# Optimization experiments

Hardware: AMD Instinct MI355X
Metric: run time of the kernel (lower is better)

## Reference

```python
import jax, jax.numpy as jnp
import numpy as np

N, E, G = 50000, 600000, 500          # nodes, edges, graphs in batch
IN_NODE, HID, EDGE = 92, 64, 41       # CGCNN default feature dims
NCONV, PRED, NOUT = 3, 128, 1
Z_DIM = 2 * HID + EDGE                # 169: cat(src_x, dst_x, edge_attr)
BN_EPS = 1e-5


def setup_inputs() -> dict:
    key = jax.random.key(0)
    ks = jax.random.split(key, 14)
    f32 = jnp.float32
    return {
        "x": jax.random.normal(ks[0], (N, IN_NODE), f32),
        "edge_attr": jax.random.normal(ks[1], (E, EDGE), f32),
        "src": jax.random.randint(ks[2], (E,), 0, N),
        "dst": jax.random.randint(ks[3], (E,), 0, N),
        "graph_idx": jnp.sort(jax.random.randint(ks[4], (N,), 0, G)),
        "n_graphs": G,
        "W_embed": jax.random.normal(ks[5], (IN_NODE, HID), f32) / np.sqrt(IN_NODE),
        "b_embed": jnp.zeros((HID,), f32),
        "W_sig": jax.random.normal(ks[6], (NCONV, Z_DIM, HID), f32) / np.sqrt(Z_DIM),
        "b_sig": jnp.zeros((NCONV, HID), f32),
        "W_sp": jax.random.normal(ks[7], (NCONV, Z_DIM, HID), f32) / np.sqrt(Z_DIM),
        "b_sp": jnp.zeros((NCONV, HID), f32),
        "bn_gamma": jnp.ones((NCONV, HID), f32),
        "bn_beta": jnp.zeros((NCONV, HID), f32),
        "W_fc": jax.random.normal(ks[8], (HID, PRED), f32) / np.sqrt(HID),
        "b_fc": jnp.zeros((PRED,), f32),
        "W_out": jax.random.normal(ks[9], (PRED, NOUT), f32) / np.sqrt(PRED),
        "b_out": jnp.zeros((NOUT,), f32),
    }


def reference(x, edge_attr, src, dst, graph_idx, n_graphs,
              W_embed, b_embed, W_sig, b_sig, W_sp, b_sp,
              bn_gamma, bn_beta, W_fc, b_fc, W_out, b_out):
    # node embedding to hidden dim
    h = x @ W_embed + b_embed                                   # [N, HID]
    n_nodes = h.shape[0]
    for i in range(W_sig.shape[0]):
        # per-edge features: gather src/dst node feats + edge feats
        z = jnp.concatenate([h[src], h[dst], edge_attr], axis=1)  # [E, Z_DIM]
        gated = jax.nn.sigmoid(z @ W_sig[i] + b_sig[i])           # [E, HID]
        msg = jax.nn.softplus(z @ W_sp[i] + b_sp[i])              # [E, HID]
        # scatter-sum gated messages into destination node mailboxes
        agg = jax.ops.segment_sum(gated * msg, dst, num_segments=n_nodes)
        h = h + agg                                               # residual
        # batch norm over nodes (training-mode batch stats, biased var)
        mean = h.mean(axis=0)
        var = h.var(axis=0)
        h = (h - mean) * jax.lax.rsqrt(var + BN_EPS) * bn_gamma[i] + bn_beta[i]
    # sum-pool nodes per graph, then dense readout
    graph_feat = jax.ops.segment_sum(h, graph_idx, num_segments=n_graphs)  # [G, HID]
    graph_feat = graph_feat @ W_fc + b_fc                                  # [G, PRED]
    return graph_feat @ W_out + b_out                                      # [G, NOUT]
```

## Files before the change

### kernel.cpp

```cpp
#include <hip/hip_runtime.h>

#define N_NODES 50000
#define N_EDGES 600000
#define N_GRAPHS 500
#define IN_F 92
#define HID 64
#define EDGE_F 41
#define ZDIM 169
#define PRED 128
#define BN_EPS 1e-5f
#define SCAN_BLOCKS 196
#define ROW_U32 24
#define LOG2E 1.4426950408889634f
#define LN2   0.6931471805599453f
#define NAGG_BLOCKS 2048
#define NW2 (NAGG_BLOCKS * 8)
#define PART_T ((N_EDGES + 1 + NW2 - 1) / NW2)

typedef unsigned int u32;
typedef _Float16 f16;
typedef _Float16 f16x2 __attribute__((ext_vector_type(2)));
typedef _Float16 f16x8 __attribute__((ext_vector_type(8)));
typedef float f32x4 __attribute__((ext_vector_type(4)));

__device__ __forceinline__ u32 f2bf(float f) {
    u32 u = __float_as_uint(f);
    return (u + 0x7fffu + ((u >> 16) & 1u)) >> 16;
}

__device__ __forceinline__ int lbound(const int* __restrict__ a, int nelem, int val) {
    int lo = 0, hi = nelem;
    while (lo < hi) {
        int m = (lo + hi) >> 1;
        if (a[m] < val) lo = m + 1; else hi = m;
    }
    return lo;
}

__global__ void k_zeroAll(int* __restrict__ ip, int n1, float* __restrict__ fp, int n2) {
    int i = blockIdx.x * 256 + threadIdx.x;
    if (i < n1) ip[i] = 0;
    else if (i - n1 < n2) fp[i - n1] = 0.f;
}

__global__ void k_hist(const int* __restrict__ dst, int* __restrict__ deg) {
    int e = blockIdx.x * 256 + threadIdx.x;
    if (e < N_EDGES) atomicAdd(&deg[dst[e]], 1);
}

__global__ __launch_bounds__(256) void k_scanA(const int* __restrict__ deg,
                                               int* __restrict__ partial) {
    __shared__ int s[256];
    int i = blockIdx.x * 256 + threadIdx.x;
    s[threadIdx.x] = (i < N_NODES) ? deg[i] : 0;
    __syncthreads();
    for (int off = 128; off > 0; off >>= 1) {
        if (threadIdx.x < off) s[threadIdx.x] += s[threadIdx.x + off];
        __syncthreads();
    }
    if (threadIdx.x == 0) partial[blockIdx.x] = s[0];
}

__global__ __launch_bounds__(256) void k_scanB(const int* __restrict__ partial,
                                               int* __restrict__ partialExc,
                                               int* __restrict__ rowptr) {
    __shared__ int s[256];
    int t = threadIdx.x;
    int v = (t < SCAN_BLOCKS) ? partial[t] : 0;
    s[t] = v;
    __syncthreads();
    for (int off = 1; off < 256; off <<= 1) {
        int x = (t >= off) ? s[t - off] : 0;
        __syncthreads();
        s[t] += x;
        __syncthreads();
    }
    partialExc[t] = s[t] - v;
    if (t == 0) rowptr[N_NODES] = N_EDGES;
}

__global__ __launch_bounds__(256) void k_scanC(const int* __restrict__ deg,
                                               const int* __restrict__ partialExc,
                                               int* __restrict__ rowptr) {
    __shared__ int s[256];
    int i = blockIdx.x * 256 + threadIdx.x;
    int t = threadIdx.x;
    int v = (i < N_NODES) ? deg[i] : 0;
    s[t] = v;
    __syncthreads();
    for (int off = 1; off < 256; off <<= 1) {
        int x = (t >= off) ? s[t - off] : 0;
        __syncthreads();
        s[t] += x;
        __syncthreads();
    }
    if (i < N_NODES) rowptr[i] = s[t] - v + partialExc[blockIdx.x];
}

__global__ void k_part(const int* __restrict__ rowptr, int* __restrict__ partW) {
    int i = blockIdx.x * 256 + threadIdx.x;
    if (i <= NW2) partW[i] = min(lbound(rowptr, N_NODES + 1, i * PART_T), N_NODES);
}

__global__ void k_rank(const int* __restrict__ dst, const int* __restrict__ src,
                       const int* __restrict__ rowptr, int* __restrict__ cursor,
                       int* __restrict__ srcS, int* __restrict__ iperm) {
    int e = blockIdx.x * 256 + threadIdx.x;
    if (e >= N_EDGES) {
        if (e < N_EDGES + 32) srcS[e] = 0;
        return;
    }
    int d = dst[e];
    int p = rowptr[d] + atomicAdd(&cursor[d], 1);
    srcS[p] = src[e];
    iperm[p] = e;
}

__global__ __launch_bounds__(256) void k_epackS(const float* __restrict__ ea,
                                                const int* __restrict__ iperm,
                                                u32* __restrict__ eapS) {
    const int total = N_EDGES * ROW_U32;
    const int stride = gridDim.x * 256;
    for (int idx = blockIdx.x * 256 + threadIdx.x; idx < total; idx += stride) {
        int p = idx / ROW_U32;
        int q = idx - p * ROW_U32;
        int e = iperm[p];
        int k0 = 2 * q, k1 = k0 + 1;
        float f0 = (k0 < EDGE_F) ? ea[(size_t)e * EDGE_F + k0] : 0.f;
        float f1 = (k1 < EDGE_F) ? ea[(size_t)e * EDGE_F + k1] : 0.f;
        f16x2 hv = {(f16)f0, (f16)f1};
        eapS[idx] = __builtin_bit_cast(u32, hv);
    }
}

__global__ void k_wprepAll(const float* __restrict__ Wsig, const float* __restrict__ Wsp,
                           const float* __restrict__ Wemb,
                           f16* __restrict__ Wf16, f16* __restrict__ Wp2,
                           f16* __restrict__ Wef) {
    int t = blockIdx.x * 256 + threadIdx.x;
    if (t < 3072) {
        int lane = t & 63;
        int jt = (t >> 6) & 7;
        int kt = (t >> 9) & 1;
        int L = t >> 10;
        int j128 = jt * 16 + (lane & 15);
        const float* Wbase = (j128 < 64) ? Wsig : Wsp;
        int j = j128 & 63;
        f16x8 v;
        #pragma unroll
        for (int b = 0; b < 8; ++b) {
            int k = kt * 32 + (lane >> 4) * 8 + b;
            float f = (k < EDGE_F) ? Wbase[(size_t)L * ZDIM * HID + (128 + k) * HID + j] * LOG2E : 0.f;
            v[b] = (f16)f;
        }
        *(f16x8*)(Wf16 + ((size_t)((L * 2 + kt) * 8 + jt) * 64 + lane) * 8) = v;
    } else if (t < 9216) {
        int t2 = t - 3072;
        int lane = t2 & 63;
        int jt = (t2 >> 6) & 15;
        int kt = (t2 >> 10) & 1;
        int L = t2 >> 11;
        int j256 = jt * 16 + (lane & 15);
        const float* Wbase = (j256 & 64) ? Wsp : Wsig;
        int rowoff = (j256 & 128) ? 64 : 0;
        int j = j256 & 63;
        f16x8 v;
        #pragma unroll
        for (int b = 0; b < 8; ++b) {
            int k = kt * 32 + (lane >> 4) * 8 + b;
            v[b] = (f16)Wbase[(size_t)L * ZDIM * HID + (rowoff + k) * HID + j];
        }
        *(f16x8*)(Wp2 + ((size_t)((L * 2 + kt) * 16 + jt) * 64 + lane) * 8) = v;
    } else if (t < 9984) {
        int t3 = t - 9216;
        int lane = t3 & 63;
        int jt = (t3 >> 6) & 3;
        int kt = t3 >> 8;
        int j = jt * 16 + (lane & 15);
        f16x8 v;
        #pragma unroll
        for (int b = 0; b < 8; ++b) {
            int k = kt * 32 + (lane >> 4) * 8 + b;
            v[b] = (k < IN_F) ? (f16)Wemb[(size_t)k * HID + j] : (f16)0.f;
        }
        *(f16x8*)(Wef + ((size_t)(kt * 4 + jt) * 64 + lane) * 8) = v;
    }
}

__global__ __launch_bounds__(256) void k_embedm(const float* __restrict__ x,
                                                const f16* __restrict__ Wef,
                                                const float* __restrict__ b,
                                                float* __restrict__ A) {
    __shared__ f16x8 Wl[12 * 64];
    for (int i = threadIdx.x; i < 12 * 64; i += 256) Wl[i] = ((const f16x8*)Wef)[i];
    __syncthreads();
    const int lane = threadIdx.x & 63;
    const int col = lane & 15, grp = lane >> 4;
    float bj[4];
    #pragma unroll
    for (int jt = 0; jt < 4; ++jt) bj[jt] = b[jt * 16 + col];
    const int wid = blockIdx.x * 4 + (threadIdx.x >> 6);
    const int nw = gridDim.x * 4;
    for (int c = wid; c < N_NODES / 16; c += nw) {
        const int node = c * 16 + col;
        const float* xr = x + (size_t)node * IN_F;
        f16x8 af[3];
        #pragma unroll
        for (int kt = 0; kt < 3; ++kt) {
            int base = kt * 32 + grp * 8;
            float4 v0 = *(const float4*)(xr + base);
            float4 v1 = (base + 4 < IN_F) ? *(const float4*)(xr + base + 4)
                                          : make_float4(0.f, 0.f, 0.f, 0.f);
            af[kt] = f16x8{(f16)v0.x, (f16)v0.y, (f16)v0.z, (f16)v0.w,
                           (f16)v1.x, (f16)v1.y, (f16)v1.z, (f16)v1.w};
        }
        #pragma unroll
        for (int jt = 0; jt < 4; ++jt) {
            f32x4 c4 = {};
            c4 = __builtin_amdgcn_mfma_f32_16x16x32_f16(af[0], Wl[(0 * 4 + jt) * 64 + lane], c4, 0, 0, 0);
            c4 = __builtin_amdgcn_mfma_f32_16x16x32_f16(af[1], Wl[(1 * 4 + jt) * 64 + lane], c4, 0, 0, 0);
            c4 = __builtin_amdgcn_mfma_f32_16x16x32_f16(af[2], Wl[(2 * 4 + jt) * 64 + lane], c4, 0, 0, 0);
            #pragma unroll
            for (int r = 0; r < 4; ++r)
                A[(size_t)(c * 16 + grp * 4 + r) * HID + jt * 16 + col] = c4[r] + bj[jt];
        }
    }
}

__global__ __launch_bounds__(256, 4) void k_projm(const float* __restrict__ A,
                                                  const float* __restrict__ statsPrev,
                                                  const float* __restrict__ gammaP,
                                                  const float* __restrict__ betaP,
                                                  int applyBN,
                                                  const f16* __restrict__ Wp2L,
                                                  const float* __restrict__ bsig,
                                                  const float* __restrict__ bsp,
                                                  u32* __restrict__ pA,
                                                  u32* __restrict__ pB,
                                                  float* __restrict__ statsOut) {
    __shared__ f16x8 Wl[32 * 64];
    for (int i = threadIdx.x; i < 32 * 64; i += 256) Wl[i] = ((const f16x8*)Wp2L)[i];
    if (blockIdx.x == 0)
        for (int i = threadIdx.x; i < 128 * 32; i += 256) statsOut[i] = 0.f;
    __syncthreads();
    const int lane = threadIdx.x & 63;
    const int col = lane & 15;
    float sck[2][8], shk[2][8];
    #pragma unroll
    for (int kt = 0; kt < 2; ++kt)
        #pragma unroll
        for (int b = 0; b < 8; ++b) {
            int k = kt * 32 + (lane >> 4) * 8 + b;
            float scv = 1.f, shv = 0.f;
            if (applyBN) {
                float m = statsPrev[k * 32] * (1.f / N_NODES);
                float v = statsPrev[(64 + k) * 32] * (1.f / N_NODES) - m * m;
                scv = rsqrtf(v + BN_EPS) * gammaP[k];
                shv = betaP[k] - m * scv;
            }
            sck[kt][b] = scv;
            shk[kt][b] = shv;
        }
    float bAs[4], bPs[4];
    #pragma unroll
    for (int jt = 0; jt < 4; ++jt) {
        bAs[jt] = bsig[jt * 16 + col] * LOG2E;
        bPs[jt] = bsp[jt * 16 + col] * LOG2E;
    }
    const int wid = blockIdx.x * 4 + (threadIdx.x >> 6);
    const int nw = gridDim.x * 4;
    for (int c = wid; c < N_NODES / 16; c += nw) {
        const int node = c * 16 + col;
        const float4* Arow = (const float4*)(A + (size_t)node * HID);
        f16x8 af[2];
        #pragma unroll
        for (int kt = 0; kt < 2; ++kt) {
            float4 v0 = Arow[kt * 8 + (lane >> 4) * 2];
            float4 v1 = Arow[kt * 8 + (lane >> 4) * 2 + 1];
            float e0 = v0.x * sck[kt][0] + shk[kt][0];
            float e1 = v0.y * sck[kt][1] + shk[kt][1];
            float e2 = v0.z * sck[kt][2] + shk[kt][2];
            float e3 = v0.w * sck[kt][3] + shk[kt][3];
            float e4 = v1.x * sck[kt][4] + shk[kt][4];
            float e5 = v1.y * sck[kt][5] + shk[kt][5];
            float e6 = v1.z * sck[kt][6] + shk[kt][6];
            float e7 = v1.w * sck[kt][7] + shk[kt][7];
            af[kt] = f16x8{(f16)e0, (f16)e1, (f16)e2, (f16)e3,
                           (f16)e4, (f16)e5, (f16)e6, (f16)e7};
        }
        #pragma unroll
        for (int h = 0; h < 2; ++h) {
            f32x4 c4[8];
            #pragma unroll
            for (int jt2 = 0; jt2 < 8; ++jt2) {
                int jt = h * 8 + jt2;
                f32x4 acc = {};
                acc = __builtin_amdgcn_mfma_f32_16x16x32_f16(af[0], Wl[(0 * 16 + jt) * 64 + lane], acc, 0, 0, 0);
                c4[jt2] = __builtin_amdgcn_mfma_f32_16x16x32_f16(af[1], Wl[(1 * 16 + jt) * 64 + lane], acc, 0, 0, 0);
            }
            u32* dstArr = h ? pB : pA;
            #pragma unroll
            for (int jt2 = 0; jt2 < 4; ++jt2)
                #pragma unroll
                for (int r = 0; r < 4; ++r) {
                    float s = fmaf(c4[jt2][r], LOG2E, h ? 0.f : bAs[jt2]);
                    float p = fmaf(c4[jt2 + 4][r], LOG2E, h ? 0.f : bPs[jt2]);
                    int n2 = c * 16 + (lane >> 4) * 4 + r;
                    dstArr[(size_t)n2 * HID + jt2 * 16 + col] = f2bf(s) | (f2bf(p) << 16);
                }
        }
    }
}


#define CTX_DECL_INIT(S, widx)                                                \
    int n##S = __builtin_amdgcn_readfirstlane(partW[widx]);                   \
    const int ne##S = __builtin_amdgcn_readfirstlane(partW[(widx) + 1]);      \
    bool act##S = n##S < ne##S;                                               \
    int rb##S = 0, re##S = 0;                                                 \
    float resid##S = 0.f;                                                     \
    float bsg##S[4], bsp##S[4], accv##S[4];                                   \
    int s0##S = 0, s1##S = 0, s2##S = 0, s3##S = 0;                           \
    {                                                                         \
        _Pragma("unroll")                                                     \
        for (int jt = 0; jt < 4; ++jt) {                                      \
            bsg##S[jt] = 0.f; bsp##S[jt] = 0.f; accv##S[jt] = 0.f;            \
        }                                                                     \
        if (act##S) {                                                         \
            rb##S = __builtin_amdgcn_readfirstlane(rowptr[n##S]);             \
            re##S = __builtin_amdgcn_readfirstlane(rowptr[n##S + 1]);         \
            resid##S = A[(size_t)n##S * HID + lane];                          \
            if (applyBN) resid##S = resid##S * scL + shL;                     \
            _Pragma("unroll")                                                 \
            for (int jt = 0; jt < 4; ++jt) {                                  \
                u32 pb = pBv[(size_t)n##S * HID + jt * 16 + col];             \
                bsg##S[jt] = __uint_as_float(pb << 16);                       \
                bsp##S[jt] = __uint_as_float(pb & 0xffff0000u);               \
            }                                                                 \
            const int* sp = srcS + rb##S + rowb;                              \
            s0##S = sp[0]; s1##S = sp[1]; s2##S = sp[2]; s3##S = sp[3];       \
        }                                                                     \
    }

#define STEP_LOADS(S)                                                         \
    u32 ga##S[4][4];                                                          \
    f16x8 a0##S, a1##S;                                                       \
    if (act##S) {                                                             \
        const u32* g0##S = pAv + (size_t)s0##S * HID + col;                   \
        const u32* g1##S = pAv + (size_t)s1##S * HID + col;                   \
        const u32* g2##S = pAv + (size_t)s2##S * HID + col;                   \
        const u32* g3##S = pAv + (size_t)s3##S * HID + col;                   \
        _Pragma("unroll")                                                     \
        for (int jt = 0; jt < 4; ++jt) {                                      \
            ga##S[jt][0] = g0##S[jt * 16];                                    \
            ga##S[jt][1] = g1##S[jt * 16];                                    \
            ga##S[jt][2] = g2##S[jt * 16];                                    \
            ga##S[jt][3] = g3##S[jt * 16];                                    \
        }                                                                     \
        const f16x8* arow##S = (const f16x8*)(eapS + (size_t)(rb##S + col) * ROW_U32); \
        a0##S = arow##S[grp];                                                 \
        a1##S = arow##S[4 + grp];                                             \
    }

#define STEP_COMPUTE(S)                                                       \
    if (act##S) {                                                             \
        const int cnt##S = re##S - rb##S;                                     \
        if (cnt##S > 0) {                                                     \
            _Pragma("unroll")                                                 \
            for (int jt = 0; jt < 4; ++jt) {                                  \
                f32x4 cs = {bsg##S[jt], bsg##S[jt], bsg##S[jt], bsg##S[jt]};  \
                f32x4 cp = {bsp##S[jt], bsp##S[jt], bsp##S[jt], bsp##S[jt]};  \
                f16x8 w0s = Wlds[(jt) * 64 + lane];                           \
                f16x8 w1s = Wlds[(8 + jt) * 64 + lane];                       \
                f16x8 w0p = Wlds[(4 + jt) * 64 + lane];                       \
                f16x8 w1p = Wlds[(12 + jt) * 64 + lane];                      \
                cs = __builtin_amdgcn_mfma_f32_16x16x32_f16(a0##S, w0s, cs, 0, 0, 0); \
                cs = __builtin_amdgcn_mfma_f32_16x16x32_f16(a1##S, w1s, cs, 0, 0, 0); \
                cp = __builtin_amdgcn_mfma_f32_16x16x32_f16(a0##S, w0p, cp, 0, 0, 0); \
                cp = __builtin_amdgcn_mfma_f32_16x16x32_f16(a1##S, w1p, cp, 0, 0, 0); \
                _Pragma("unroll")                                             \
                for (int r = 0; r < 4; ++r) {                                 \
                    float s_ = cs[r] + __uint_as_float(ga##S[jt][r] << 16);   \
                    float p_ = cp[r] + __uint_as_float(ga##S[jt][r] & 0xffff0000u); \
                    float g_ = __builtin_amdgcn_rcpf(1.f + exp2f(-s_));       \
                    float m_ = fmaxf(p_, 0.f) + log2f(1.f + exp2f(-fabsf(p_))); \
                    accv##S[jt] += (rowb + r < cnt##S) ? g_ * m_ : 0.f;       \
                }                                                             \
            }                                                                 \
            rb##S += 16;                                                      \
        }                                                                     \
        while (rb##S >= re##S) {                                              \
            _Pragma("unroll")                                                 \
            for (int jt = 0; jt < 4; ++jt) {                                  \
                accv##S[jt] += __shfl_xor(accv##S[jt], 16);                   \
                accv##S[jt] += __shfl_xor(accv##S[jt], 32);                   \
            }                                                                 \
            float accSel = (lane & 32) ? ((lane & 16) ? accv##S[3] : accv##S[2]) \
                                       : ((lane & 16) ? accv##S[1] : accv##S[0]); \
            float outv = resid##S + accSel * LN2;                             \
            Aout[(size_t)n##S * HID + lane] = outv;                           \
            lsum += outv;                                                     \
            lsq += outv * outv;                                               \
            accv##S[0] = accv##S[1] = accv##S[2] = accv##S[3] = 0.f;          \
            rb##S = re##S;                                                    \
            ++n##S;                                                           \
            if (n##S >= ne##S) { act##S = false; break; }                     \
            re##S = __builtin_amdgcn_readfirstlane(rowptr[n##S + 1]);         \
            resid##S = A[(size_t)n##S * HID + lane];                          \
            if (applyBN) resid##S = resid##S * scL + shL;                     \
            _Pragma("unroll")                                                 \
            for (int jt = 0; jt < 4; ++jt) {                                  \
                u32 pb = pBv[(size_t)n##S * HID + jt * 16 + col];             \
                bsg##S[jt] = __uint_as_float(pb << 16);                       \
                bsp##S[jt] = __uint_as_float(pb & 0xffff0000u);               \
            }                                                                 \
        }                                                                     \
        if (act##S) {                                                         \
            const int* sp##S = srcS + rb##S + rowb;                           \
            s0##S = sp##S[0]; s1##S = sp##S[1];                               \
            s2##S = sp##S[2]; s3##S = sp##S[3];                               \
        }                                                                     \
    }

__global__ __launch_bounds__(256, 4) void k_nodeagg(const float* __restrict__ A,
                                                    const float* __restrict__ statsPrev,
                                                    const float* __restrict__ gammaP,
                                                    const float* __restrict__ betaP,
                                                    int applyBN,
                                                    const u32* __restrict__ pAv,
                                                    const u32* __restrict__ pBv,
                                                    const u32* __restrict__ eapS,
                                                    const int* __restrict__ srcS,
                                                    const int* __restrict__ rowptr,
                                                    const int* __restrict__ partW,
                                                    const f16* __restrict__ Wf16L,
                                                    float* __restrict__ Aout,
                                                    float* __restrict__ statsOut) {
    __shared__ f16x8 Wlds[16 * 64];
    __shared__ float redS[256], redQ[256];
    for (int i = threadIdx.x; i < 16 * 64; i += 256)
        Wlds[i] = ((const f16x8*)Wf16L)[i];

    const int lane = threadIdx.x & 63;
    const int col = lane & 15;
    const int grp = lane >> 4;
    const int rowb = grp * 4;

    float scL = 1.f, shL = 0.f;
    if (applyBN) {
        float m = statsPrev[lane * 32] * (1.f / N_NODES);
        float v = statsPrev[(64 + lane) * 32] * (1.f / N_NODES) - m * m;
        scL = rsqrtf(v + BN_EPS) * gammaP[lane];
        shL = betaP[lane] - m * scL;
    }
    __syncthreads();

    const int w2 = (((blockIdx.x << 2) + (threadIdx.x >> 6)) << 1);
    float lsum = 0.f, lsq = 0.f;

    CTX_DECL_INIT(A, w2)
    CTX_DECL_INIT(B, w2 + 1)

    while (actA || actB) {
        STEP_LOADS(A)
        STEP_LOADS(B)
        STEP_COMPUTE(A)
        STEP_COMPUTE(B)
    }

    redS[threadIdx.x] = lsum;
    redQ[threadIdx.x] = lsq;
    __syncthreads();
    if (threadIdx.x < 64) {
        float s = redS[threadIdx.x] + redS[threadIdx.x + 64] + redS[threadIdx.x + 128] + redS[threadIdx.x + 192];
        float q = redQ[threadIdx.x] + redQ[threadIdx.x + 64] + redQ[threadIdx.x + 128] + redQ[threadIdx.x + 192];
        unsafeAtomicAdd(&statsOut[threadIdx.x * 32], s);
        unsafeAtomicAdd(&statsOut[(64 + threadIdx.x) * 32], q);
    }
}

__global__ __launch_bounds__(256) void k_poolbn(const float* __restrict__ A,
                                                const float* __restrict__ stats,
                                                const float* __restrict__ gamma,
                                                const float* __restrict__ beta,
                                                const int* __restrict__ gidx,
                                                float* __restrict__ gf) {
    const int lane = threadIdx.x & 63;
    float m = stats[lane * 32] * (1.f / N_NODES);
    float v = stats[(64 + lane) * 32] * (1.f / N_NODES) - m * m;
    float scv = rsqrtf(v + BN_EPS) * gamma[lane];
    float shv = beta[lane] - m * scv;
    const int wid = blockIdx.x * 4 + (threadIdx.x >> 6);
    const int nwaves = gridDim.x * 4;
    const int chunk = (N_NODES + nwaves - 1) / nwaves;
    int r0 = wid * chunk;
    if (r0 >= N_NODES) return;
    int r1 = min(r0 + chunk, N_NODES);
    int gcur = gidx[r0];
    float acc = 0.f;
    for (int r = r0; r < r1; ++r) {
        int g = gidx[r];
        if (g != gcur) {
            unsafeAtomicAdd(&gf[(size_t)gcur * HID + lane], acc);
            acc = 0.f;
            gcur = g;
        }
        acc += A[(size_t)r * HID + lane] * scv + shv;
    }
    unsafeAtomicAdd(&gf[(size_t)gcur * HID + lane], acc);
}

__global__ __launch_bounds__(256) void k_readout(const float* __restrict__ gf,
                                                 const float* __restrict__ Wfc,
                                                 const float* __restrict__ bfc,
                                                 const float* __restrict__ Wout,
                                                 const float* __restrict__ bout,
                                                 float* __restrict__ out) {
    const int lane = threadIdx.x & 63;
    const int g = blockIdx.x * 4 + (threadIdx.x >> 6);
    if (g >= N_GRAPHS) return;
    const float* row = gf + (size_t)g * HID;
    float p0 = bfc[lane], p1 = bfc[64 + lane];
    #pragma unroll 4
    for (int k = 0; k < HID; ++k) {
        float v = row[k];
        p0 += v * Wfc[k * PRED + lane];
        p1 += v * Wfc[k * PRED + 64 + lane];
    }
    float part = p0 * Wout[lane] + p1 * Wout[64 + lane];
    #pragma unroll
    for (int off = 32; off > 0; off >>= 1) part += __shfl_xor(part, off);
    if (lane == 0) out[g] = part + bout[0];
}

extern "C" void kernel_launch(void* const* d_in, const int* in_sizes, int n_in,
                              void* d_out, int out_size, void* d_ws, size_t ws_size,
                              hipStream_t stream) {
    const float* x         = (const float*)d_in[0];
    const float* edge_attr = (const float*)d_in[1];
    const int*   src       = (const int*)d_in[2];
    const int*   dst       = (const int*)d_in[3];
    const int*   gidx      = (const int*)d_in[4];
    const float* W_embed   = (const float*)d_in[6];
    const float* b_embed   = (const float*)d_in[7];
    const float* W_sig     = (const float*)d_in[8];
    const float* b_sig     = (const float*)d_in[9];
    const float* W_sp      = (const float*)d_in[10];
    const float* b_sp      = (const float*)d_in[11];
    const float* bn_gamma  = (const float*)d_in[12];
    const float* bn_beta   = (const float*)d_in[13];
    const float* W_fc      = (const float*)d_in[14];
    const float* b_fc      = (const float*)d_in[15];
    const float* W_out     = (const float*)d_in[16];
    const float* b_out     = (const float*)d_in[17];
    float* out = (float*)d_out;

    const size_t NH = (size_t)N_NODES * HID;
    float* ws     = (float*)d_ws;
    float* A      = ws;
    u32*   pA     = (u32*)(A + NH);
    u32*   pB     = pA + NH;
    u32*   eapS   = pB + NH;
    int*   srcS   = (int*)(eapS + (size_t)(N_EDGES + 32) * ROW_U32);
    int*   iperm  = srcS + N_EDGES + 32;
    int*   rowptr = iperm + N_EDGES;
    int*   deg    = rowptr + N_NODES + 1;
    int*   cursor = deg + N_NODES;
    int*   partial    = cursor + N_NODES;
    int*   partialExc = partial + 256;
    int*   partW  = partialExc + 256;
    f16*   Wf16   = (f16*)(partW + NW2 + 2);
    f16*   Wp2    = Wf16 + 3 * 2 * 8 * 64 * 8;
    f16*   Wef    = Wp2 + 3 * 2 * 16 * 64 * 8;
    float* stats  = (float*)(Wef + 3 * 4 * 64 * 8);
    float* gf     = stats + 3 * 4096;

    k_wprepAll<<<39, 256, 0, stream>>>(W_sig, W_sp, W_embed, Wf16, Wp2, Wef);
    k_zeroAll<<<(2 * N_NODES + N_GRAPHS * HID + 255) / 256, 256, 0, stream>>>(
        deg, 2 * N_NODES, gf, N_GRAPHS * HID);
    k_hist<<<(N_EDGES + 255) / 256, 256, 0, stream>>>(dst, deg);
    k_scanA<<<SCAN_BLOCKS, 256, 0, stream>>>(deg, partial);
    k_scanB<<<1, 256, 0, stream>>>(partial, partialExc, rowptr);
    k_scanC<<<SCAN_BLOCKS, 256, 0, stream>>>(deg, partialExc, rowptr);
    k_part<<<(NW2 + 1 + 255) / 256, 256, 0, stream>>>(rowptr, partW);
    k_rank<<<(N_EDGES + 32 + 255) / 256, 256, 0, stream>>>(dst, src, rowptr, cursor, srcS, iperm);
    k_embedm<<<512, 256, 0, stream>>>(x, Wef, b_embed, A);
    k_epackS<<<4096, 256, 0, stream>>>(edge_attr, iperm, eapS);

    for (int i = 0; i < 3; ++i) {
        const float* stPrev = stats + (size_t)(i > 0 ? i - 1 : 0) * 4096;
        const float* gP     = bn_gamma + (i > 0 ? i - 1 : 0) * HID;
        const float* bP     = bn_beta + (i > 0 ? i - 1 : 0) * HID;
        float* stOut        = stats + (size_t)i * 4096;
        int applyBN = (i > 0) ? 1 : 0;
        k_projm<<<512, 256, 0, stream>>>(A, stPrev, gP, bP, applyBN,
                                         Wp2 + (size_t)i * 2 * 16 * 64 * 8,
                                         b_sig + i * HID, b_sp + i * HID,
                                         pA, pB, stOut);
        k_nodeagg<<<NAGG_BLOCKS, 256, 0, stream>>>(A, stPrev, gP, bP, applyBN,
                                                   pA, pB, eapS, srcS, rowptr, partW,
                                                   Wf16 + (size_t)i * 2 * 8 * 64 * 8,
                                                   A, stOut);
    }

    k_poolbn<<<256, 256, 0, stream>>>(A, stats + 2 * 4096, bn_gamma + 2 * HID,
                                      bn_beta + 2 * HID, gidx, gf);
    k_readout<<<(N_GRAPHS + 3) / 4, 256, 0, stream>>>(gf, W_fc, b_fc, W_out, b_out, out);
}
```

Before: 528.9 us.

## Vectorize bf16 pair layout, fuse prep/partition kernels, merge pool+readout per graph

```diff
diff --git a/kernel.cpp b/kernel.cpp
--- a/kernel.cpp
+++ b/kernel.cpp
@@ -28,6 +28,10 @@
     return (u + 0x7fffu + ((u >> 16) & 1u)) >> 16;
 }
 
+__device__ __forceinline__ u32 vget(uint4 v, int i) {
+    switch (i) { case 0: return v.x; case 1: return v.y; case 2: return v.z; default: return v.w; }
+}
+
 __device__ __forceinline__ int lbound(const int* __restrict__ a, int nelem, int val) {
     int lo = 0, hi = nelem;
     while (lo < hi) {
@@ -37,10 +41,64 @@
     return lo;
 }
 
-__global__ void k_zeroAll(int* __restrict__ ip, int n1, float* __restrict__ fp, int n2) {
-    int i = blockIdx.x * 256 + threadIdx.x;
-    if (i < n1) ip[i] = 0;
-    else if (i - n1 < n2) fp[i - n1] = 0.f;
+__global__ void k_prep(const float* __restrict__ Wsig, const float* __restrict__ Wsp,
+                       const float* __restrict__ Wemb, const int* __restrict__ gidx,
+                       f16* __restrict__ Wf16, f16* __restrict__ Wp2,
+                       f16* __restrict__ Wef, int* __restrict__ gstart,
+                       int* __restrict__ zeroBase) {
+    int t = blockIdx.x * 256 + threadIdx.x;
+    if (t < 3072) {
+        int lane = t & 63;
+        int jt = (t >> 6) & 7;
+        int kt = (t >> 9) & 1;
+        int L = t >> 10;
+        int j128 = jt * 16 + (lane & 15);
+        const float* Wbase = (j128 < 64) ? Wsig : Wsp;
+        int j = j128 & 63;
+        f16x8 v;
+        #pragma unroll
+        for (int b = 0; b < 8; ++b) {
+            int k = kt * 32 + (lane >> 4) * 8 + b;
+            float f = (k < EDGE_F) ? Wbase[(size_t)L * ZDIM * HID + (128 + k) * HID + j] * LOG2E : 0.f;
+            v[b] = (f16)f;
+        }
+        *(f16x8*)(Wf16 + ((size_t)((L * 2 + kt) * 8 + jt) * 64 + lane) * 8) = v;
+    } else if (t < 9216) {
+        int t2 = t - 3072;
+        int lane = t2 & 63;
+        int jt = (t2 >> 6) & 15;
+        int kt = (t2 >> 10) & 1;
+        int L = t2 >> 11;
+        int j256 = jt * 16 + (lane & 15);
+        const float* Wbase = (j256 & 64) ? Wsp : Wsig;
+        int rowoff = (j256 & 128) ? 64 : 0;
+        int j = j256 & 63;
+        f16x8 v;
+        #pragma unroll
+        for (int b = 0; b < 8; ++b) {
+            int k = kt * 32 + (lane >> 4) * 8 + b;
+            v[b] = (f16)Wbase[(size_t)L * ZDIM * HID + (rowoff + k) * HID + j];
+        }
+        *(f16x8*)(Wp2 + ((size_t)((L * 2 + kt) * 16 + jt) * 64 + lane) * 8) = v;
+    } else if (t < 9984) {
+        int t3 = t - 9216;
+        int lane = t3 & 63;
+        int jt = (t3 >> 6) & 3;
+        int kt = t3 >> 8;
+        int j = jt * 16 + (lane & 15);
+        f16x8 v;
+        #pragma unroll
+        for (int b = 0; b < 8; ++b) {
+            int k = kt * 32 + (lane >> 4) * 8 + b;
+            v[b] = (k < IN_F) ? (f16)Wemb[(size_t)k * HID + j] : (f16)0.f;
+        }
+        *(f16x8*)(Wef + ((size_t)(kt * 4 + jt) * 64 + lane) * 8) = v;
+    } else if (t < 10485) {
+        int g = t - 9984;
+        gstart[g] = lbound(gidx, N_NODES, g);
+    } else if (t < 10485 + 2 * N_NODES) {
+        zeroBase[t - 10485] = 0;
+    }
 }
 
 __global__ void k_hist(const int* __restrict__ dst, int* __restrict__ deg) {
@@ -97,15 +155,12 @@
     if (i < N_NODES) rowptr[i] = s[t] - v + partialExc[blockIdx.x];
 }
 
-__global__ void k_part(const int* __restrict__ rowptr, int* __restrict__ partW) {
-    int i = blockIdx.x * 256 + threadIdx.x;
-    if (i <= NW2) partW[i] = min(lbound(rowptr, N_NODES + 1, i * PART_T), N_NODES);
-}
-
 __global__ void k_rank(const int* __restrict__ dst, const int* __restrict__ src,
                        const int* __restrict__ rowptr, int* __restrict__ cursor,
-                       int* __restrict__ srcS, int* __restrict__ iperm) {
+                       int* __restrict__ srcS, int* __restrict__ iperm,
+                       int* __restrict__ partW) {
     int e = blockIdx.x * 256 + threadIdx.x;
+    if (e <= NW2) partW[e] = min(lbound(rowptr, N_NODES + 1, e * PART_T), N_NODES);
     if (e >= N_EDGES) {
         if (e < N_EDGES + 32) srcS[e] = 0;
         return;
@@ -130,60 +185,6 @@
         float f1 = (k1 < EDGE_F) ? ea[(size_t)e * EDGE_F + k1] : 0.f;
         f16x2 hv = {(f16)f0, (f16)f1};
         eapS[idx] = __builtin_bit_cast(u32, hv);
-    }
-}
-
-__global__ void k_wprepAll(const float* __restrict__ Wsig, const float* __restrict__ Wsp,
-                           const float* __restrict__ Wemb,
-                           f16* __restrict__ Wf16, f16* __restrict__ Wp2,
-                           f16* __restrict__ Wef) {
-    int t = blockIdx.x * 256 + threadIdx.x;
-    if (t < 3072) {
-        int lane = t & 63;
-        int jt = (t >> 6) & 7;
-        int kt = (t >> 9) & 1;
-        int L = t >> 10;
-        int j128 = jt * 16 + (lane & 15);
-        const float* Wbase = (j128 < 64) ? Wsig : Wsp;
-        int j = j128 & 63;
-        f16x8 v;
-        #pragma unroll
-        for (int b = 0; b < 8; ++b) {
-            int k = kt * 32 + (lane >> 4) * 8 + b;
-            float f = (k < EDGE_F) ? Wbase[(size_t)L * ZDIM * HID + (128 + k) * HID + j] * LOG2E : 0.f;
-            v[b] = (f16)f;
-        }
-        *(f16x8*)(Wf16 + ((size_t)((L * 2 + kt) * 8 + jt) * 64 + lane) * 8) = v;
-    } else if (t < 9216) {
-        int t2 = t - 3072;
-        int lane = t2 & 63;
-        int jt = (t2 >> 6) & 15;
-        int kt = (t2 >> 10) & 1;
-        int L = t2 >> 11;
-        int j256 = jt * 16 + (lane & 15);
-        const float* Wbase = (j256 & 64) ? Wsp : Wsig;
-        int rowoff = (j256 & 128) ? 64 : 0;
-        int j = j256 & 63;
-        f16x8 v;
-        #pragma unroll
-        for (int b = 0; b < 8; ++b) {
-            int k = kt * 32 + (lane >> 4) * 8 + b;
-            v[b] = (f16)Wbase[(size_t)L * ZDIM * HID + (rowoff + k) * HID + j];
-        }
-        *(f16x8*)(Wp2 + ((size_t)((L * 2 + kt) * 16 + jt) * 64 + lane) * 8) = v;
-    } else if (t < 9984) {
-        int t3 = t - 9216;
-        int lane = t3 & 63;
-        int jt = (t3 >> 6) & 3;
-        int kt = t3 >> 8;
-        int j = jt * 16 + (lane & 15);
-        f16x8 v;
-        #pragma unroll
-        for (int b = 0; b < 8; ++b) {
-            int k = kt * 32 + (lane >> 4) * 8 + b;
-            v[b] = (k < IN_F) ? (f16)Wemb[(size_t)k * HID + j] : (f16)0.f;
-        }
-        *(f16x8*)(Wef + ((size_t)(kt * 4 + jt) * 64 + lane) * 8) = v;
     }
 }
 
@@ -300,18 +301,21 @@
             }
             u32* dstArr = h ? pB : pA;
             #pragma unroll
-            for (int jt2 = 0; jt2 < 4; ++jt2)
+            for (int r = 0; r < 4; ++r) {
+                uint4 q;
+                u32* qp = (u32*)&q;
                 #pragma unroll
-                for (int r = 0; r < 4; ++r) {
+                for (int jt2 = 0; jt2 < 4; ++jt2) {
                     float s = fmaf(c4[jt2][r], LOG2E, h ? 0.f : bAs[jt2]);
                     float p = fmaf(c4[jt2 + 4][r], LOG2E, h ? 0.f : bPs[jt2]);
-                    int n2 = c * 16 + (lane >> 4) * 4 + r;
-                    dstArr[(size_t)n2 * HID + jt2 * 16 + col] = f2bf(s) | (f2bf(p) << 16);
+                    qp[jt2] = f2bf(s) | (f2bf(p) << 16);
                 }
-        }
-    }
-}
-
+                int n2 = c * 16 + (lane >> 4) * 4 + r;
+                *(uint4*)(dstArr + (size_t)n2 * HID + col * 4) = q;
+            }
+        }
+    }
+}
 
 #define CTX_DECL_INIT(S, widx)                                                \
     int n##S = __builtin_amdgcn_readfirstlane(partW[widx]);                   \
@@ -331,11 +335,12 @@
             re##S = __builtin_amdgcn_readfirstlane(rowptr[n##S + 1]);         \
             resid##S = A[(size_t)n##S * HID + lane];                          \
             if (applyBN) resid##S = resid##S * scL + shL;                     \
+            uint4 pb = *(const uint4*)(pBv + (size_t)n##S * HID + col * 4);   \
             _Pragma("unroll")                                                 \
             for (int jt = 0; jt < 4; ++jt) {                                  \
-                u32 pb = pBv[(size_t)n##S * HID + jt * 16 + col];             \
-                bsg##S[jt] = __uint_as_float(pb << 16);                       \
-                bsp##S[jt] = __uint_as_float(pb & 0xffff0000u);               \
+                u32 w_ = vget(pb, jt);                                        \
+                bsg##S[jt] = __uint_as_float(w_ << 16);                       \
+                bsp##S[jt] = __uint_as_float(w_ & 0xffff0000u);               \
             }                                                                 \
             const int* sp = srcS + rb##S + rowb;                              \
             s0##S = sp[0]; s1##S = sp[1]; s2##S = sp[2]; s3##S = sp[3];       \
@@ -343,52 +348,41 @@
     }
 
 #define STEP_LOADS(S)                                                         \
-    u32 ga##S[4][4];                                                          \
+    uint4 ga4##S[4];                                                          \
     f16x8 a0##S, a1##S;                                                       \
     if (act##S) {                                                             \
-        const u32* g0##S = pAv + (size_t)s0##S * HID + col;                   \
-        const u32* g1##S = pAv + (size_t)s1##S * HID + col;                   \
-        const u32* g2##S = pAv + (size_t)s2##S * HID + col;                   \
-        const u32* g3##S = pAv + (size_t)s3##S * HID + col;                   \
-        _Pragma("unroll")                                                     \
-        for (int jt = 0; jt < 4; ++jt) {                                      \
-            ga##S[jt][0] = g0##S[jt * 16];                                    \
-            ga##S[jt][1] = g1##S[jt * 16];                                    \
-            ga##S[jt][2] = g2##S[jt * 16];                                    \
-            ga##S[jt][3] = g3##S[jt * 16];                                    \
-        }                                                                     \
+        ga4##S[0] = *(const uint4*)(pAv + (size_t)s0##S * HID + col * 4);     \
+        ga4##S[1] = *(const uint4*)(pAv + (size_t)s1##S * HID + col * 4);     \
+        ga4##S[2] = *(const uint4*)(pAv + (size_t)s2##S * HID + col * 4);     \
+        ga4##S[3] = *(const uint4*)(pAv + (size_t)s3##S * HID + col * 4);     \
         const f16x8* arow##S = (const f16x8*)(eapS + (size_t)(rb##S + col) * ROW_U32); \
         a0##S = arow##S[grp];                                                 \
         a1##S = arow##S[4 + grp];                                             \
     }
 
-#define STEP_COMPUTE(S)                                                       \
+#define CTX_JT(S, jt)                                                         \
     if (act##S) {                                                             \
-        const int cnt##S = re##S - rb##S;                                     \
-        if (cnt##S > 0) {                                                     \
-            _Pragma("unroll")                                                 \
-            for (int jt = 0; jt < 4; ++jt) {                                  \
-                f32x4 cs = {bsg##S[jt], bsg##S[jt], bsg##S[jt], bsg##S[jt]};  \
-                f32x4 cp = {bsp##S[jt], bsp##S[jt], bsp##S[jt], bsp##S[jt]};  \
-                f16x8 w0s = Wlds[(jt) * 64 + lane];                           \
-                f16x8 w1s = Wlds[(8 + jt) * 64 + lane];                       \
-                f16x8 w0p = Wlds[(4 + jt) * 64 + lane];                       \
-                f16x8 w1p = Wlds[(12 + jt) * 64 + lane];                      \
-                cs = __builtin_amdgcn_mfma_f32_16x16x32_f16(a0##S, w0s, cs, 0, 0, 0); \
-                cs = __builtin_amdgcn_mfma_f32_16x16x32_f16(a1##S, w1s, cs, 0, 0, 0); \
-                cp = __builtin_amdgcn_mfma_f32_16x16x32_f16(a0##S, w0p, cp, 0, 0, 0); \
-                cp = __builtin_amdgcn_mfma_f32_16x16x32_f16(a1##S, w1p, cp, 0, 0, 0); \
-                _Pragma("unroll")                                             \
-                for (int r = 0; r < 4; ++r) {                                 \
-                    float s_ = cs[r] + __uint_as_float(ga##S[jt][r] << 16);   \
-                    float p_ = cp[r] + __uint_as_float(ga##S[jt][r] & 0xffff0000u); \
-                    float g_ = __builtin_amdgcn_rcpf(1.f + exp2f(-s_));       \
-                    float m_ = fmaxf(p_, 0.f) + log2f(1.f + exp2f(-fabsf(p_))); \
-                    accv##S[jt] += (rowb + r < cnt##S) ? g_ * m_ : 0.f;       \
-                }                                                             \
-            }                                                                 \
-            rb##S += 16;                                                      \
+        f32x4 cs = {bsg##S[jt], bsg##S[jt], bsg##S[jt], bsg##S[jt]};          \
+        f32x4 cp = {bsp##S[jt], bsp##S[jt], bsp##S[jt], bsp##S[jt]};          \
+        cs = __builtin_amdgcn_mfma_f32_16x16x32_f16(a0##S, w0s, cs, 0, 0, 0); \
+        cs = __builtin_amdgcn_mfma_f32_16x16x32_f16(a1##S, w1s, cs, 0, 0, 0); \
+        cp = __builtin_amdgcn_mfma_f32_16x16x32_f16(a0##S, w0p, cp, 0, 0, 0); \
+        cp = __builtin_amdgcn_mfma_f32_16x16x32_f16(a1##S, w1p, cp, 0, 0, 0); \
+        const int cnt = re##S - rb##S;                                        \
+        _Pragma("unroll")                                                     \
+        for (int r = 0; r < 4; ++r) {                                         \
+            u32 gw = vget(ga4##S[r], jt);                                     \
+            float s_ = cs[r] + __uint_as_float(gw << 16);                     \
+            float p_ = cp[r] + __uint_as_float(gw & 0xffff0000u);             \
+            float g_ = __builtin_amdgcn_rcpf(1.f + exp2f(-s_));               \
+            float m_ = fmaxf(p_, 0.f) + log2f(1.f + exp2f(-fabsf(p_)));       \
+            accv##S[jt] += (rowb + r < cnt) ? g_ * m_ : 0.f;                  \
         }                                                                     \
+    }
+
+#define CTX_ADVANCE(S)                                                        \
+    if (act##S) {                                                             \
+        rb##S += 16;                                                          \
         while (rb##S >= re##S) {                                              \
             _Pragma("unroll")                                                 \
             for (int jt = 0; jt < 4; ++jt) {                                  \
@@ -408,11 +402,12 @@
             re##S = __builtin_amdgcn_readfirstlane(rowptr[n##S + 1]);         \
             resid##S = A[(size_t)n##S * HID + lane];                          \
             if (applyBN) resid##S = resid##S * scL + shL;                     \
+            uint4 pb = *(const uint4*)(pBv + (size_t)n##S * HID + col * 4);   \
             _Pragma("unroll")                                                 \
             for (int jt = 0; jt < 4; ++jt) {                                  \
-                u32 pb = pBv[(size_t)n##S * HID + jt * 16 + col];             \
-                bsg##S[jt] = __uint_as_float(pb << 16);                       \
-                bsp##S[jt] = __uint_as_float(pb & 0xffff0000u);               \
+                u32 w_ = vget(pb, jt);                                        \
+                bsg##S[jt] = __uint_as_float(w_ << 16);                       \
+                bsp##S[jt] = __uint_as_float(w_ & 0xffff0000u);               \
             }                                                                 \
         }                                                                     \
         if (act##S) {                                                         \
@@ -464,8 +459,17 @@
     while (actA || actB) {
         STEP_LOADS(A)
         STEP_LOADS(B)
-        STEP_COMPUTE(A)
-        STEP_COMPUTE(B)
+        #pragma unroll
+        for (int jt = 0; jt < 4; ++jt) {
+            f16x8 w0s = Wlds[jt * 64 + lane];
+            f16x8 w1s = Wlds[(8 + jt) * 64 + lane];
+            f16x8 w0p = Wlds[(4 + jt) * 64 + lane];
+            f16x8 w1p = Wlds[(12 + jt) * 64 + lane];
+            CTX_JT(A, jt)
+            CTX_JT(B, jt)
+        }
+        CTX_ADVANCE(A)
+        CTX_ADVANCE(B)
     }
 
     redS[threadIdx.x] = lsum;
@@ -479,58 +483,49 @@
     }
 }
 
-__global__ __launch_bounds__(256) void k_poolbn(const float* __restrict__ A,
-                                                const float* __restrict__ stats,
-                                                const float* __restrict__ gamma,
-                                                const float* __restrict__ beta,
-                                                const int* __restrict__ gidx,
-                                                float* __restrict__ gf) {
-    const int lane = threadIdx.x & 63;
-    float m = stats[lane * 32] * (1.f / N_NODES);
-    float v = stats[(64 + lane) * 32] * (1.f / N_NODES) - m * m;
-    float scv = rsqrtf(v + BN_EPS) * gamma[lane];
-    float shv = beta[lane] - m * scv;
-    const int wid = blockIdx.x * 4 + (threadIdx.x >> 6);
-    const int nwaves = gridDim.x * 4;
-    const int chunk = (N_NODES + nwaves - 1) / nwaves;
-    int r0 = wid * chunk;
-    if (r0 >= N_NODES) return;
-    int r1 = min(r0 + chunk, N_NODES);
-    int gcur = gidx[r0];
-    float acc = 0.f;
-    for (int r = r0; r < r1; ++r) {
-        int g = gidx[r];
-        if (g != gcur) {
-            unsafeAtomicAdd(&gf[(size_t)gcur * HID + lane], acc);
-            acc = 0.f;
-            gcur = g;
-        }
-        acc += A[(size_t)r * HID + lane] * scv + shv;
-    }
-    unsafeAtomicAdd(&gf[(size_t)gcur * HID + lane], acc);
-}
-
-__global__ __launch_bounds__(256) void k_readout(const float* __restrict__ gf,
+__global__ __launch_bounds__(256) void k_poolout(const float* __restrict__ A,
+                                                 const float* __restrict__ stats,
+                                                 const float* __restrict__ gamma,
+                                                 const float* __restrict__ beta,
+                                                 const int* __restrict__ gstart,
                                                  const float* __restrict__ Wfc,
                                                  const float* __restrict__ bfc,
                                                  const float* __restrict__ Wout,
                                                  const float* __restrict__ bout,
                                                  float* __restrict__ out) {
+    const int g = blockIdx.x;
     const int lane = threadIdx.x & 63;
-    const int g = blockIdx.x * 4 + (threadIdx.x >> 6);
-    if (g >= N_GRAPHS) return;
-    const float* row = gf + (size_t)g * HID;
-    float p0 = bfc[lane], p1 = bfc[64 + lane];
-    #pragma unroll 4
-    for (int k = 0; k < HID; ++k) {
-        float v = row[k];
-        p0 += v * Wfc[k * PRED + lane];
-        p1 += v * Wfc[k * PRED + 64 + lane];
-    }
-    float part = p0 * Wout[lane] + p1 * Wout[64 + lane];
-    #pragma unroll
-    for (int off = 32; off > 0; off >>= 1) part += __shfl_xor(part, off);
-    if (lane == 0) out[g] = part + bout[0];
+    const int wv = threadIdx.x >> 6;
+    const int rb = gstart[g], re = gstart[g + 1];
+    float s = 0.f;
+    for (int r = rb + wv; r < re; r += 4) s += A[(size_t)r * HID + lane];
+    __shared__ float red[4][64];
+    __shared__ float gfeat[64];
+    red[wv][lane] = s;
+    __syncthreads();
+    if (threadIdx.x < 64) {
+        float t = red[0][lane] + red[1][lane] + red[2][lane] + red[3][lane];
+        float m = stats[lane * 32] * (1.f / N_NODES);
+        float v = stats[(64 + lane) * 32] * (1.f / N_NODES) - m * m;
+        float scv = rsqrtf(v + BN_EPS) * gamma[lane];
+        float shv = beta[lane] - m * scv;
+        gfeat[lane] = scv * t + shv * (float)(re - rb);
+    }
+    __syncthreads();
+    __shared__ float r2[128];
+    if (threadIdx.x < 128) {
+        float p = bfc[threadIdx.x];
+        #pragma unroll 8
+        for (int k = 0; k < 64; ++k) p += gfeat[k] * Wfc[k * PRED + threadIdx.x];
+        r2[threadIdx.x] = p * Wout[threadIdx.x];
+    }
+    __syncthreads();
+    if (threadIdx.x < 64) {
+        float v2 = r2[threadIdx.x] + r2[threadIdx.x + 64];
+        #pragma unroll
+        for (int off = 32; off > 0; off >>= 1) v2 += __shfl_down(v2, off);
+        if (threadIdx.x == 0) out[g] = v2 + bout[0];
+    }
 }
 
 extern "C" void kernel_launch(void* const* d_in, const int* in_sizes, int n_in,
@@ -569,21 +564,20 @@
     int*   partial    = cursor + N_NODES;
     int*   partialExc = partial + 256;
     int*   partW  = partialExc + 256;
-    f16*   Wf16   = (f16*)(partW + NW2 + 2);
+    int*   gstart = partW + NW2 + 2;
+    f16*   Wf16   = (f16*)(((size_t)(gstart + 504) + 15) & ~(size_t)15);
     f16*   Wp2    = Wf16 + 3 * 2 * 8 * 64 * 8;
     f16*   Wef    = Wp2 + 3 * 2 * 16 * 64 * 8;
     float* stats  = (float*)(Wef + 3 * 4 * 64 * 8);
-    float* gf     = stats + 3 * 4096;
-
-    k_wprepAll<<<39, 256, 0, stream>>>(W_sig, W_sp, W_embed, Wf16, Wp2, Wef);
-    k_zeroAll<<<(2 * N_NODES + N_GRAPHS * HID + 255) / 256, 256, 0, stream>>>(
-        deg, 2 * N_NODES, gf, N_GRAPHS * HID);
+
+    k_prep<<<(10485 + 2 * N_NODES + 255) / 256, 256, 0, stream>>>(
+        W_sig, W_sp, W_embed, gidx, Wf16, Wp2, Wef, gstart, deg);
     k_hist<<<(N_EDGES + 255) / 256, 256, 0, stream>>>(dst, deg);
     k_scanA<<<SCAN_BLOCKS, 256, 0, stream>>>(deg, partial);
     k_scanB<<<1, 256, 0, stream>>>(partial, partialExc, rowptr);
     k_scanC<<<SCAN_BLOCKS, 256, 0, stream>>>(deg, partialExc, rowptr);
-    k_part<<<(NW2 + 1 + 255) / 256, 256, 0, stream>>>(rowptr, partW);
-    k_rank<<<(N_EDGES + 32 + 255) / 256, 256, 0, stream>>>(dst, src, rowptr, cursor, srcS, iperm);
+    k_rank<<<(N_EDGES + 32 + 255) / 256, 256, 0, stream>>>(dst, src, rowptr, cursor,
+                                                           srcS, iperm, partW);
     k_embedm<<<512, 256, 0, stream>>>(x, Wef, b_embed, A);
     k_epackS<<<4096, 256, 0, stream>>>(edge_attr, iperm, eapS);
 
@@ -603,7 +597,7 @@
                                                    A, stOut);
     }
 
-    k_poolbn<<<256, 256, 0, stream>>>(A, stats + 2 * 4096, bn_gamma + 2 * HID,
-                                      bn_beta + 2 * HID, gidx, gf);
-    k_readout<<<(N_GRAPHS + 3) / 4, 256, 0, stream>>>(gf, W_fc, b_fc, W_out, b_out, out);
-}
+    k_poolout<<<N_GRAPHS, 256, 0, stream>>>(A, stats + 2 * 4096, bn_gamma + 2 * HID,
+                                            bn_beta + 2 * HID, gstart,
+                                            W_fc, b_fc, W_out, b_out, out);
+}
```

Measured after the change: 799.0 us. +51.1%, slower.
